# Kernel tuning notes

Measured on AMD Instinct MI355X. Metric: run time of the kernel, lower is better.

The kernel has to match this reference:

```python
import jax, jax.numpy as jnp
import numpy as np

N_QUBITS = 8      # kernel_size == n wires
N_LAYERS = 4
OUT_CHANNELS = 8
STRIDE = 1


def _ry(state, theta, wire):
    """Apply RY(theta) on `wire`. state: (P, 2,2,...,2) real; theta scalar or (P,)."""
    axis = wire + 1
    a0 = jnp.take(state, 0, axis=axis)
    a1 = jnp.take(state, 1, axis=axis)
    half = theta * 0.5
    c, s = jnp.cos(half), jnp.sin(half)
    # broadcast per-patch angles over remaining qubit axes
    extra = a0.ndim - jnp.ndim(c)
    if extra > 0:
        c = jnp.reshape(c, jnp.shape(c) + (1,) * extra)
        s = jnp.reshape(s, jnp.shape(s) + (1,) * extra)
    return jnp.stack([c * a0 - s * a1, s * a0 + c * a1], axis=axis)


def _cnot(state, ctrl, tgt):
    ca, ta = ctrl + 1, tgt + 1
    c0 = jnp.take(state, 0, axis=ca)
    c1 = jnp.take(state, 1, axis=ca)
    ta_adj = ta - 1 if ta > ca else ta  # target axis index after removing ctrl axis
    c1 = jnp.flip(c1, axis=ta_adj)      # X on target where ctrl==1
    return jnp.stack([c0, c1], axis=ca)


def _circuit(patches, w):
    """Batched statevector simulation. patches: (P, N_QUBITS); w: (N_LAYERS*N_QUBITS,).
    RY/CNOT on a real |0...0> keep the state real -> float32 statevector."""
    P = patches.shape[0]
    state = jnp.zeros((P,) + (2,) * N_QUBITS, dtype=patches.dtype)
    state = state.at[(slice(None),) + (0,) * N_QUBITS].set(1.0)
    # AngleEmbedding: RY(pi * x_q) on wire q
    for q in range(N_QUBITS):
        state = _ry(state, patches[:, q] * jnp.pi, q)
    for layer in range(N_LAYERS):
        for q in range(N_QUBITS):
            state = _ry(state, w[layer * N_QUBITS + q], q)
        for q in range(N_QUBITS - 1):
            state = _cnot(state, q, q + 1)
    # <Z x Z x ... x Z> = sum |amp|^2 * (-1)^parity(bits)
    z = jnp.array([1.0, -1.0], dtype=state.dtype)
    sign = z
    for _ in range(N_QUBITS - 1):
        sign = sign[..., None] * z
    return jnp.sum(state * state * sign, axis=tuple(range(1, N_QUBITS + 1)))


def setup_inputs() -> dict:
    key = jax.random.key(0)
    k1, k2 = jax.random.split(key)
    x = jax.random.uniform(k1, (128, 1, 512), dtype=jnp.float32)
    weights = jax.random.uniform(k2, (OUT_CHANNELS, N_LAYERS * N_QUBITS), dtype=jnp.float32) * (2.0 * jnp.pi)
    return {"x": x, "weights": weights}


def reference(x, weights):
    B, _, L = x.shape
    out_L = (L - N_QUBITS) // STRIDE + 1
    # gather all sliding-window patches at once: (B, out_L, K) -> (B*out_L, K)
    idx = jnp.arange(out_L)[:, None] * STRIDE + jnp.arange(N_QUBITS)[None, :]
    patches = x[:, 0, idx].reshape(B * out_L, N_QUBITS)
    outs = [_circuit(patches, weights[k]) for k in range(OUT_CHANNELS)]
    out = jnp.stack(outs, axis=0).reshape(OUT_CHANNELS, B, out_L)
    return jnp.transpose(out, (1, 0, 2))  # (B, C_out, out_L)
```

## Files before the change

kernel.cpp:

```cpp
#include <hip/hip_runtime.h>
#include <math.h>

#define NQ       8
#define NLAYERS  4
#define OUTC     8
#define BATCH    128
#define LEN      512
#define OUTL     505
#define NPATCH   (BATCH * OUTL)
#define BM       64
#define NBLK     (NPATCH / BM)
#define BLK_PER_CH 1010

typedef __attribute__((ext_vector_type(8))) short bf16x8;
typedef __attribute__((ext_vector_type(4))) float f32x4;

__device__ __forceinline__ ushort to_bf16(float f) {
    union { float f; unsigned int u; } v; v.f = f;
    unsigned int b = v.u + 0x7FFFu + ((v.u >> 16) & 1u);
    return (ushort)(b >> 16);
}

__device__ __forceinline__ unsigned pk_bf16(float lo, float hi) {
    unsigned r;
    asm("v_cvt_pk_bf16_f32 %0, %1, %2" : "=v"(r) : "v"(lo), "v"(hi));
    return r;
}

template <int CTRL>
__device__ __forceinline__ float dpp_xor(float x) {
    int i = __float_as_int(x);
    int r = __builtin_amdgcn_update_dpp(0, i, CTRL, 0xF, 0xF, true);
    return __int_as_float(r);
}

template <int N>
__device__ __forceinline__ float ror_add(float x) {
    int i = __float_as_int(x);
    int r = __builtin_amdgcn_update_dpp(0, i, 0x120 + N, 0xF, 0xF, true);
    return x + __int_as_float(r);
}

__device__ __forceinline__ void run_layers(float st[64], const float* wk, int b0, int b7) {
#pragma unroll 1
    for (int layer = 0; layer < NLAYERS; ++layer) {
        float wc[NQ], wsn[NQ];
#pragma unroll
        for (int q = 0; q < NQ; ++q) {
            float half = 0.5f * wk[layer * NQ + q];
            wc[q]  = __cosf(half);
            wsn[q] = __sinf(half);
        }
        {
            const float sg = b0 ? wsn[0] : -wsn[0];
#pragma unroll
            for (int r = 0; r < 64; ++r) {
                float p = dpp_xor<0x4E>(st[r]);
                st[r] = fmaf(wc[0], st[r], sg * p);
            }
        }
#pragma unroll
        for (int q = 1; q <= 6; ++q) {
            const int m = 1 << (6 - q);
#pragma unroll
            for (int r = 0; r < 64; ++r) {
                if (r & m) continue;
                float a0 = st[r], a1 = st[r + m];
                st[r]     = fmaf(wc[q], a0, -wsn[q] * a1);
                st[r + m] = fmaf(wc[q], a1,  wsn[q] * a0);
            }
        }
        {
            const float sg = b7 ? wsn[7] : -wsn[7];
#pragma unroll
            for (int r = 0; r < 64; ++r) {
                float p = dpp_xor<0xB1>(st[r]);
                st[r] = fmaf(wc[7], st[r], sg * p);
            }
        }
#pragma unroll
        for (int r = 0; r < 32; ++r) {
            float t0 = st[r], t1 = st[r + 32];
            st[r]      = b0 ? t1 : t0;
            st[r + 32] = b0 ? t0 : t1;
        }
#pragma unroll
        for (int q = 1; q <= 5; ++q) {
            const int cm = 1 << (6 - q);
            const int tm = 1 << (5 - q);
#pragma unroll
            for (int r = 0; r < 64; ++r) {
                if ((r & cm) && !(r & tm)) {
                    float t = st[r]; st[r] = st[r + tm]; st[r + tm] = t;
                }
            }
        }
#pragma unroll
        for (int r = 1; r < 64; r += 2) st[r] = dpp_xor<0xB1>(st[r]);
    }
}

__global__ __launch_bounds__(256) void build_m(const float* __restrict__ w,
                                               ushort* __restrict__ W2) {
    const int tid  = threadIdx.x;
    const int lane = tid & 63;
    const int k    = blockIdx.x >> 2;
    const int j    = ((blockIdx.x & 3) << 6) | (tid >> 2);
    const int b0 = (lane >> 1) & 1;
    const int b7 = lane & 1;

    float st[64];
    const int r0 = (j >> 1) & 63;
    const bool mine = (b0 == ((j >> 7) & 1)) && (b7 == (j & 1));
#pragma unroll
    for (int r = 0; r < 64; ++r) st[r] = (mine && r == r0) ? 1.0f : 0.0f;

    run_layers(st, w + k * (NLAYERS * NQ), b0, b7);

    const int ph = (k << 3) | (j >> 5);
    const int gj = (j >> 3) & 3;
    const int je = j & 7;
#pragma unroll
    for (int r = 0; r < 64; ++r) {
        int i  = (b0 << 7) | (r << 1) | b7;
        size_t idx = (size_t)((ph * 4 + (i >> 6)) * 4 + ((i >> 4) & 3)) * 512
                   + (gj * 16 + (i & 15)) * 8 + je;
        W2[idx] = to_bf16(st[r]);
    }
}

__global__ __launch_bounds__(256, 2) void qconv_mfma(const float* __restrict__ x,
                                                     const ushort* __restrict__ W2,
                                                     float* __restrict__ out) {
    __shared__ ushort Alds[64 * 256];
    __shared__ float  red[OUTC * 4 * 64];

    const int tid  = threadIdx.x;
    const int lane = tid & 63;
    const int wv   = tid >> 6;
    const int u    = lane & 15;
    const int g    = lane >> 4;
    const int pbase = blockIdx.x * BM;

    const ushort* bbase = W2 + (size_t)wv * 2048 + lane * 8;

    uint4 breg[2][4];
#pragma unroll
    for (int pp = 0; pp < 2; ++pp)
#pragma unroll
        for (int ct = 0; ct < 4; ++ct)
            breg[pp][ct] = *(const uint4*)(bbase + pp * 8192 + ct * 512);

    {
        const int row = lane;
        const int jb  = wv;
        const int p = pbase + row;
        const int b = p / OUTL, ol = p - b * OUTL;
        const float* xp = x + b * LEN + ol;
        float ec[NQ], es[NQ];
#pragma unroll
        for (int q = 0; q < NQ; ++q) {
            float half = xp[q] * 1.5707963267948966f;
            ec[q] = __cosf(half);
            es[q] = __sinf(half);
        }
        float st[64];
        st[0] = (jb & 2 ? es[0] : ec[0]) * (jb & 1 ? es[1] : ec[1]);
#pragma unroll
        for (int q = 2; q <= 7; ++q) {
            const int m = 1 << (7 - q);
#pragma unroll
            for (int jj = (1 << (q - 2)) - 1; jj >= 0; --jj) {
                float v = st[jj * 2 * m];
                st[jj * 2 * m + m] = v * es[q];
                st[jj * 2 * m]     = v * ec[q];
            }
        }
#pragma unroll
        for (int cc = 0; cc < 8; ++cc) {
            uint4 vv;
            vv.x = pk_bf16(st[cc * 8 + 0], st[cc * 8 + 1]);
            vv.y = pk_bf16(st[cc * 8 + 2], st[cc * 8 + 3]);
            vv.z = pk_bf16(st[cc * 8 + 4], st[cc * 8 + 5]);
            vv.w = pk_bf16(st[cc * 8 + 6], st[cc * 8 + 7]);
            int phys = ((jb * 8 + cc) ^ (row & 7)) & 31;
            *(uint4*)((char*)Alds + row * 512 + phys * 16) = vv;
        }
    }
    __syncthreads();

    const int pu = __builtin_popcount(u) & 1;
    const int pw = __builtin_popcount(wv) & 1;

#pragma unroll 1
    for (int ch = 0; ch < 8; ++ch) {
        f32x4 acc[4][4];
#pragma unroll
        for (int a = 0; a < 4; ++a)
#pragma unroll
            for (int c = 0; c < 4; ++c) acc[a][c] = (f32x4){0.f, 0.f, 0.f, 0.f};

#pragma unroll
        for (int s = 0; s < 8; ++s) {
            const int slot = s & 1;
#pragma unroll
            for (int rt = 0; rt < 4; ++rt) {
                int row = rt * 16 + u;
                int phys = ((s * 4 + g) ^ (row & 7)) & 31;
                bf16x8 af = *(const bf16x8*)((const char*)Alds + row * 512 + phys * 16);
#pragma unroll
                for (int ct = 0; ct < 4; ++ct)
                    acc[rt][ct] = __builtin_amdgcn_mfma_f32_16x16x32_bf16(
                        af, *(bf16x8*)&breg[slot][ct], acc[rt][ct], 0, 0, 0);
            }
            const int phn = ch * 8 + s + 2;
            if (s < 6 || ch < 7) {
#pragma unroll
                for (int ct = 0; ct < 4; ++ct)
                    breg[slot][ct] = *(const uint4*)(bbase + phn * 8192 + ct * 512);
            }
        }

#pragma unroll
        for (int rt = 0; rt < 4; ++rt) {
            f32x4 part = (f32x4){0.f, 0.f, 0.f, 0.f};
#pragma unroll
            for (int ct = 0; ct < 4; ++ct) {
                float sgn = ((pu + pw + __builtin_popcount(ct)) & 1) ? -1.0f : 1.0f;
                part += (acc[rt][ct] * acc[rt][ct]) * sgn;
            }
            float v0 = part[0], v1 = part[1], v2 = part[2], v3 = part[3];
            v0 = ror_add<8>(ror_add<4>(ror_add<2>(ror_add<1>(v0))));
            v1 = ror_add<8>(ror_add<4>(ror_add<2>(ror_add<1>(v1))));
            v2 = ror_add<8>(ror_add<4>(ror_add<2>(ror_add<1>(v2))));
            v3 = ror_add<8>(ror_add<4>(ror_add<2>(ror_add<1>(v3))));
            if (u == 0) {
                f32x4 vv = (f32x4){v0, v1, v2, v3};
                *(f32x4*)&red[(ch * 4 + wv) * 64 + rt * 16 + g * 4] = vv;
            }
        }
    }

    __syncthreads();
#pragma unroll
    for (int e = 0; e < 2; ++e) {
        int idx = tid + e * 256;
        int ch = idx >> 6, row = idx & 63;
        float o = red[(ch * 4 + 0) * 64 + row] + red[(ch * 4 + 1) * 64 + row] +
                  red[(ch * 4 + 2) * 64 + row] + red[(ch * 4 + 3) * 64 + row];
        int p = pbase + row;
        int b = p / OUTL, ol = p - b * OUTL;
        out[b * (OUTC * OUTL) + ch * OUTL + ol] = o;
    }
}

__global__ __launch_bounds__(256) void qconv_direct(const float* __restrict__ x,
                                                    const float* __restrict__ w,
                                                    float* __restrict__ out) {
    const int lane = threadIdx.x & 63;
    const int wave = threadIdx.x >> 6;
    const int bi   = blockIdx.x;
    const int k    = bi / BLK_PER_CH;
    const int pblk = bi % BLK_PER_CH;
    const int patch = pblk * 64 + wave * 16 + (lane >> 2);
    const int b0 = (lane >> 1) & 1;
    const int b7 = lane & 1;
    const int b  = patch / OUTL;
    const int ol = patch - b * OUTL;
    const float* xp = x + b * LEN + ol;

    float ec[NQ], es[NQ];
#pragma unroll
    for (int q = 0; q < NQ; ++q) {
        float half = xp[q] * 1.5707963267948966f;
        ec[q] = __cosf(half);
        es[q] = __sinf(half);
    }
    float st[64];
    st[0] = (b0 ? es[0] : ec[0]) * (b7 ? es[7] : ec[7]);
#pragma unroll
    for (int q = 1; q <= 6; ++q) {
        const int m = 1 << (6 - q);
#pragma unroll
        for (int j = (1 << (q - 1)) - 1; j >= 0; --j) {
            float v = st[j * 2 * m];
            st[j * 2 * m + m] = v * es[q];
            st[j * 2 * m]     = v * ec[q];
        }
    }
    run_layers(st, w + k * (NLAYERS * NQ), b0, b7);

    float accp = 0.0f, accm = 0.0f;
#pragma unroll
    for (int r = 0; r < 64; ++r) {
        if (__builtin_popcount(r) & 1) accm = fmaf(st[r], st[r], accm);
        else                           accp = fmaf(st[r], st[r], accp);
    }
    float v = accp - accm;
    if (b0 ^ b7) v = -v;
    v += dpp_xor<0xB1>(v);
    v += dpp_xor<0x4E>(v);
    if ((lane & 3) == 0) out[b * (OUTC * OUTL) + k * OUTL + ol] = v;
}

extern "C" void kernel_launch(void* const* d_in, const int* in_sizes, int n_in,
                              void* d_out, int out_size, void* d_ws, size_t ws_size,
                              hipStream_t stream) {
    const float* x = (const float*)d_in[0];
    const float* w = (const float*)d_in[1];
    float* out = (float*)d_out;

    if (ws_size < (size_t)(8 * 256 * 256 * 2)) {
        qconv_direct<<<dim3(OUTC * BLK_PER_CH), 256, 0, stream>>>(x, w, out);
        return;
    }
    ushort* W2 = (ushort*)d_ws;
    build_m<<<dim3(32), 256, 0, stream>>>(w, W2);
    qconv_mfma<<<dim3(NBLK), 256, 0, stream>>>(x, W2, out);
}
```

Before: 83.56 us.

## Split MFMA work across eight waves per block with half the column tiles each

The MFMA kernel now launches 512 threads (8 waves) per 64-patch block instead of 4. Each wave owns half as many column tiles and builds a 32-entry slice of the embedded state. The per-wave accumulators and B-register buffers shrink by half. This is meant to cut register pressure and raise the waves available to hide B-fragment load latency. In exchange it adds a larger LDS reduction buffer and an 8-way final sum, and the launch-bounds occupancy hint is dropped.

```diff
diff --git a/kernel.cpp b/kernel.cpp
--- a/kernel.cpp
+++ b/kernel.cpp
@@ -129,11 +129,11 @@
     }
 }
 
-__global__ __launch_bounds__(256, 2) void qconv_mfma(const float* __restrict__ x,
-                                                     const ushort* __restrict__ W2,
-                                                     float* __restrict__ out) {
+__global__ __launch_bounds__(512) void qconv_mfma(const float* __restrict__ x,
+                                                  const ushort* __restrict__ W2,
+                                                  float* __restrict__ out) {
     __shared__ ushort Alds[64 * 256];
-    __shared__ float  red[OUTC * 4 * 64];
+    __shared__ float  red[OUTC * 8 * 64];
 
     const int tid  = threadIdx.x;
     const int lane = tid & 63;
@@ -142,18 +142,17 @@
     const int g    = lane >> 4;
     const int pbase = blockIdx.x * BM;
 
-    const ushort* bbase = W2 + (size_t)wv * 2048 + lane * 8;
-
-    uint4 breg[2][4];
+    const ushort* bbase = W2 + (size_t)wv * 1024 + lane * 8;
+
+    uint4 breg[2][2];
 #pragma unroll
     for (int pp = 0; pp < 2; ++pp)
 #pragma unroll
-        for (int ct = 0; ct < 4; ++ct)
+        for (int ct = 0; ct < 2; ++ct)
             breg[pp][ct] = *(const uint4*)(bbase + pp * 8192 + ct * 512);
 
     {
         const int row = lane;
-        const int jb  = wv;
         const int p = pbase + row;
         const int b = p / OUTL, ol = p - b * OUTL;
         const float* xp = x + b * LEN + ol;
@@ -164,41 +163,42 @@
             ec[q] = __cosf(half);
             es[q] = __sinf(half);
         }
-        float st[64];
-        st[0] = (jb & 2 ? es[0] : ec[0]) * (jb & 1 ? es[1] : ec[1]);
-#pragma unroll
-        for (int q = 2; q <= 7; ++q) {
+        float st[32];
+        st[0] = (wv & 4 ? es[0] : ec[0]) * (wv & 2 ? es[1] : ec[1])
+              * (wv & 1 ? es[2] : ec[2]);
+#pragma unroll
+        for (int q = 3; q <= 7; ++q) {
             const int m = 1 << (7 - q);
 #pragma unroll
-            for (int jj = (1 << (q - 2)) - 1; jj >= 0; --jj) {
+            for (int jj = (1 << (q - 3)) - 1; jj >= 0; --jj) {
                 float v = st[jj * 2 * m];
                 st[jj * 2 * m + m] = v * es[q];
                 st[jj * 2 * m]     = v * ec[q];
             }
         }
 #pragma unroll
-        for (int cc = 0; cc < 8; ++cc) {
+        for (int cc = 0; cc < 4; ++cc) {
             uint4 vv;
             vv.x = pk_bf16(st[cc * 8 + 0], st[cc * 8 + 1]);
             vv.y = pk_bf16(st[cc * 8 + 2], st[cc * 8 + 3]);
             vv.z = pk_bf16(st[cc * 8 + 4], st[cc * 8 + 5]);
             vv.w = pk_bf16(st[cc * 8 + 6], st[cc * 8 + 7]);
-            int phys = ((jb * 8 + cc) ^ (row & 7)) & 31;
+            int phys = ((wv * 4 + cc) ^ (row & 7)) & 31;
             *(uint4*)((char*)Alds + row * 512 + phys * 16) = vv;
         }
     }
     __syncthreads();
 
-    const int pu = __builtin_popcount(u) & 1;
-    const int pw = __builtin_popcount(wv) & 1;
+    const float slane = ((__builtin_popcount(wv) + __builtin_popcount(u)) & 1)
+                        ? -1.0f : 1.0f;
 
 #pragma unroll 1
     for (int ch = 0; ch < 8; ++ch) {
-        f32x4 acc[4][4];
+        f32x4 acc[4][2];
 #pragma unroll
         for (int a = 0; a < 4; ++a)
 #pragma unroll
-            for (int c = 0; c < 4; ++c) acc[a][c] = (f32x4){0.f, 0.f, 0.f, 0.f};
+            for (int c = 0; c < 2; ++c) acc[a][c] = (f32x4){0.f, 0.f, 0.f, 0.f};
 
 #pragma unroll
         for (int s = 0; s < 8; ++s) {
@@ -209,26 +209,21 @@
                 int phys = ((s * 4 + g) ^ (row & 7)) & 31;
                 bf16x8 af = *(const bf16x8*)((const char*)Alds + row * 512 + phys * 16);
 #pragma unroll
-                for (int ct = 0; ct < 4; ++ct)
+                for (int ct = 0; ct < 2; ++ct)
                     acc[rt][ct] = __builtin_amdgcn_mfma_f32_16x16x32_bf16(
                         af, *(bf16x8*)&breg[slot][ct], acc[rt][ct], 0, 0, 0);
             }
             const int phn = ch * 8 + s + 2;
             if (s < 6 || ch < 7) {
 #pragma unroll
-                for (int ct = 0; ct < 4; ++ct)
-                    breg[slot][ct] = *(const uint4*)(bbase + phn * 8192 + ct * 512);
+                for (int ct = 0; ct < 2; ++ct)
+                    breg[slot][ct] = *(const uint4*)(bbase + (size_t)phn * 8192 + ct * 512);
             }
         }
 
 #pragma unroll
         for (int rt = 0; rt < 4; ++rt) {
-            f32x4 part = (f32x4){0.f, 0.f, 0.f, 0.f};
-#pragma unroll
-            for (int ct = 0; ct < 4; ++ct) {
-                float sgn = ((pu + pw + __builtin_popcount(ct)) & 1) ? -1.0f : 1.0f;
-                part += (acc[rt][ct] * acc[rt][ct]) * sgn;
-            }
+            f32x4 part = (acc[rt][0] * acc[rt][0] - acc[rt][1] * acc[rt][1]) * slane;
             float v0 = part[0], v1 = part[1], v2 = part[2], v3 = part[3];
             v0 = ror_add<8>(ror_add<4>(ror_add<2>(ror_add<1>(v0))));
             v1 = ror_add<8>(ror_add<4>(ror_add<2>(ror_add<1>(v1))));
@@ -236,18 +231,17 @@
             v3 = ror_add<8>(ror_add<4>(ror_add<2>(ror_add<1>(v3))));
             if (u == 0) {
                 f32x4 vv = (f32x4){v0, v1, v2, v3};
-                *(f32x4*)&red[(ch * 4 + wv) * 64 + rt * 16 + g * 4] = vv;
+                *(f32x4*)&red[(ch * 8 + wv) * 64 + rt * 16 + g * 4] = vv;
             }
         }
     }
 
     __syncthreads();
-#pragma unroll
-    for (int e = 0; e < 2; ++e) {
-        int idx = tid + e * 256;
-        int ch = idx >> 6, row = idx & 63;
-        float o = red[(ch * 4 + 0) * 64 + row] + red[(ch * 4 + 1) * 64 + row] +
-                  red[(ch * 4 + 2) * 64 + row] + red[(ch * 4 + 3) * 64 + row];
+    {
+        int ch = tid >> 6, row = tid & 63;
+        float o = 0.0f;
+#pragma unroll
+        for (int w8 = 0; w8 < 8; ++w8) o += red[(ch * 8 + w8) * 64 + row];
         int p = pbase + row;
         int b = p / OUTL, ol = p - b * OUTL;
         out[b * (OUTC * OUTL) + ch * OUTL + ol] = o;
@@ -316,5 +310,5 @@
     }
     ushort* W2 = (ushort*)d_ws;
     build_m<<<dim3(32), 256, 0, stream>>>(w, W2);
-    qconv_mfma<<<dim3(NBLK), 256, 0, stream>>>(x, W2, out);
-}
+    qconv_mfma<<<dim3(NBLK), 512, 0, stream>>>(x, W2, out);
+}
```

After: 88.36 us. 5.7% more time.
